# Optimization experiments

Measured on AMD Instinct MI355X. Metric: run time of the kernel, lower is better.

Reference implementation:

```python
import jax, jax.numpy as jnp
import numpy as np

HEADS = 16
DIM_HEAD = 64
SEG = 512        # segment_len (block-diagonal window)
P = 16           # num persistent memory tokens


def rmsnorm(x, g, eps=1e-6):
    var = jnp.mean(x * x, axis=-1, keepdims=True)
    return x * jax.lax.rsqrt(var + eps) * g


def setup_inputs() -> dict:
    key = jax.random.key(0)
    ks = jax.random.split(key, 6)
    B, S, D = 2, 4096, 1024
    inner = HEADS * DIM_HEAD
    return {
        "x": jax.random.normal(ks[0], (B, S, D), jnp.float32),
        "gamma": jnp.ones((D,), jnp.float32),
        "w_qkv": jax.random.normal(ks[1], (D, inner * 3), jnp.float32) * (D ** -0.5),
        "w_out": jax.random.normal(ks[2], (inner, D), jnp.float32) * (inner ** -0.5),
        "pm_k": jax.random.normal(ks[3], (HEADS, P, DIM_HEAD), jnp.float32) * 0.02,
        "pm_v": jax.random.normal(ks[4], (HEADS, P, DIM_HEAD), jnp.float32) * 0.02,
    }


def reference(x, gamma, w_qkv, w_out, pm_k, pm_v):
    # SegmentedAttention forward (MAC block-diagonal causal + persistent memory)
    B, S, D = x.shape
    pad = (-S) % SEG
    Sp = S + pad
    nw = Sp // SEG

    h = rmsnorm(x, gamma)
    qkv = h @ w_qkv                              # [B, S, 3*inner]
    q, k, v = jnp.split(qkv, 3, axis=-1)

    def fold(t):
        # pad and fold segments into batch: b (w n) (h d) -> b w h n d
        t = jnp.pad(t, ((0, 0), (0, pad), (0, 0)))
        t = t.reshape(B, nw, SEG, HEADS, DIM_HEAD)
        return t.transpose(0, 1, 3, 2, 4)        # [B, W, H, SEG, Dh]

    q, k, v = fold(q), fold(k), fold(v)

    # persistent memory tokens prepended to every segment's k/v
    pmk = jnp.broadcast_to(pm_k, (B, nw, HEADS, P, DIM_HEAD))
    pmv = jnp.broadcast_to(pm_v, (B, nw, HEADS, P, DIM_HEAD))
    k = jnp.concatenate([pmk, k], axis=3)        # [B, W, H, P+SEG, Dh]
    v = jnp.concatenate([pmv, v], axis=3)

    scale = DIM_HEAD ** -0.5
    sim = jnp.einsum('bwhid,bwhjd->bwhij', q, k) * scale  # [B,W,H,SEG,P+SEG]

    # mask: persistent mem always visible; within-segment causal (block
    # diagonality is implicit from folding segments into batch)
    qi = jnp.arange(SEG)[:, None]
    kj = jnp.arange(SEG + P)[None, :] - P
    mask = (kj < 0) | (qi >= kj)
    sim = jnp.where(mask, sim, -jnp.inf)

    attn = jax.nn.softmax(sim, axis=-1)
    out = jnp.einsum('bwhij,bwhjd->bwhid', attn, v)       # [B,W,H,SEG,Dh]
    out = out.transpose(0, 1, 3, 2, 4).reshape(B, Sp, HEADS * DIM_HEAD)
    out = out[:, :S]
    return out @ w_out
```

## Files before the change

### kernel.cpp

```cpp
#include <hip/hip_runtime.h>

typedef __attribute__((ext_vector_type(8))) short short8;
typedef __attribute__((ext_vector_type(4))) float float4v;

#define SEG 512
#define PMEM 16
#define NKEY 528

__device__ __forceinline__ float b2f(unsigned int u) {
    union { unsigned int i; float f; } v; v.i = u << 16; return v.f;
}
__device__ __forceinline__ unsigned short f2b(float f) {
    union { float f; unsigned int i; } v; v.f = f;
    unsigned int b = v.i;
    return (unsigned short)((b + 0x7FFFu + ((b >> 16) & 1u)) >> 16);
}

__device__ __forceinline__ int detect_bf16(const void* gamma) {
    return ((const unsigned short*)gamma)[0] == 0x3F80u;
}

__device__ __forceinline__ void async_ld16(const unsigned short* g, unsigned short* l) {
    __builtin_amdgcn_global_load_lds(
        (const __attribute__((address_space(1))) void*)g,
        (__attribute__((address_space(3))) void*)l,
        16, 0, 0);
}

__global__ __launch_bounds__(256) void prep_k(
    const void* __restrict__ w_qkv, const void* __restrict__ w_out,
    const void* __restrict__ pm_k, const void* __restrict__ pm_v,
    const void* __restrict__ x, const void* __restrict__ gamma,
    unsigned short* __restrict__ wqkvT, unsigned short* __restrict__ woutT,
    unsigned short* __restrict__ pmkb, unsigned short* __restrict__ pmvb,
    unsigned short* __restrict__ h) {
    int f = detect_bf16(gamma);
    int bidx = blockIdx.x;
    int tid = threadIdx.x;
    if (bidx < 4096) {
        __shared__ unsigned short t[32][33];
        const void* in; unsigned short* out; int R, C, bx, by;
        if (bidx < 3072) {
            in = w_qkv; out = wqkvT; R = 1024; C = 3072;
            bx = (bidx % 96) * 32; by = (bidx / 96) * 32;
        } else {
            int t2 = bidx - 3072;
            in = w_out; out = woutT; R = 1024; C = 1024;
            bx = (t2 & 31) * 32; by = (t2 >> 5) * 32;
        }
        const unsigned short* in16 = (const unsigned short*)in;
        const float* in32 = (const float*)in;
        int tx = tid & 31, ty = tid >> 5;
        #pragma unroll
        for (int j = 0; j < 32; j += 8) {
            long idx = (long)(by + ty + j) * C + bx + tx;
            t[ty + j][tx] = f ? in16[idx] : f2b(in32[idx]);
        }
        __syncthreads();
        #pragma unroll
        for (int j = 0; j < 32; j += 8)
            out[(long)(bx + ty + j) * R + by + tx] = t[tx][ty + j];
    } else if (bidx < 4104) {
        int i = (bidx - 4096) * 2048 + tid * 8;
        if (f) {
            *(uint4*)(pmkb + i) = *(const uint4*)((const unsigned short*)pm_k + i);
            *(uint4*)(pmvb + i) = *(const uint4*)((const unsigned short*)pm_v + i);
        } else {
            const float* pk = (const float*)pm_k + i;
            const float* pv = (const float*)pm_v + i;
            uint4 kd, vd;
            float4 k0 = *(const float4*)pk, k1 = *(const float4*)(pk + 4);
            float4 v0 = *(const float4*)pv, v1 = *(const float4*)(pv + 4);
            kd.x = (unsigned int)f2b(k0.x) | ((unsigned int)f2b(k0.y) << 16);
            kd.y = (unsigned int)f2b(k0.z) | ((unsigned int)f2b(k0.w) << 16);
            kd.z = (unsigned int)f2b(k1.x) | ((unsigned int)f2b(k1.y) << 16);
            kd.w = (unsigned int)f2b(k1.z) | ((unsigned int)f2b(k1.w) << 16);
            vd.x = (unsigned int)f2b(v0.x) | ((unsigned int)f2b(v0.y) << 16);
            vd.y = (unsigned int)f2b(v0.z) | ((unsigned int)f2b(v0.w) << 16);
            vd.z = (unsigned int)f2b(v1.x) | ((unsigned int)f2b(v1.y) << 16);
            vd.w = (unsigned int)f2b(v1.z) | ((unsigned int)f2b(v1.w) << 16);
            *(uint4*)(pmkb + i) = kd;
            *(uint4*)(pmvb + i) = vd;
        }
    } else {
        __shared__ float wsum[4];
        long row = bidx - 4104;
        float f0, f1, f2, f3, g0, g1, g2, g3;
        if (f) {
            const unsigned short* xp = (const unsigned short*)x;
            const unsigned short* gp = (const unsigned short*)gamma;
            uint2 xv = *(const uint2*)(xp + row * 1024 + tid * 4);
            f0 = b2f(xv.x & 0xffffu); f1 = b2f(xv.x >> 16);
            f2 = b2f(xv.y & 0xffffu); f3 = b2f(xv.y >> 16);
            uint2 gv = *(const uint2*)(gp + tid * 4);
            g0 = b2f(gv.x & 0xffffu); g1 = b2f(gv.x >> 16);
            g2 = b2f(gv.y & 0xffffu); g3 = b2f(gv.y >> 16);
        } else {
            const float* xp = (const float*)x;
            const float* gp = (const float*)gamma;
            float4 xv = *(const float4*)(xp + row * 1024 + tid * 4);
            f0 = xv.x; f1 = xv.y; f2 = xv.z; f3 = xv.w;
            float4 gv = *(const float4*)(gp + tid * 4);
            g0 = gv.x; g1 = gv.y; g2 = gv.z; g3 = gv.w;
        }
        float ss = f0 * f0 + f1 * f1 + f2 * f2 + f3 * f3;
        #pragma unroll
        for (int off = 1; off < 64; off <<= 1) ss += __shfl_xor(ss, off, 64);
        int lane = tid & 63, wv = tid >> 6;
        if (lane == 0) wsum[wv] = ss;
        __syncthreads();
        float tot = wsum[0] + wsum[1] + wsum[2] + wsum[3];
        float sc = rsqrtf(tot * (1.0f / 1024.0f) + 1e-6f);
        uint2 o;
        o.x = (unsigned int)f2b(f0 * sc * g0) | ((unsigned int)f2b(f1 * sc * g1) << 16);
        o.y = (unsigned int)f2b(f2 * sc * g2) | ((unsigned int)f2b(f3 * sc * g3) << 16);
        *(uint2*)(h + row * 1024 + tid * 4) = o;
    }
}

__global__ __launch_bounds__(256, 4) void gemm_bt(
    const unsigned short* __restrict__ A, const unsigned short* __restrict__ Bt,
    void* __restrict__ Cv, int M, int N, int K,
    const void* __restrict__ gamma, int out_mode) {
    __shared__ unsigned short SM[16384];
    unsigned short* As = SM;
    unsigned short* Bs = SM + 8192;
    int out_bf16 = out_mode == 0 ? 1 : detect_bf16(gamma);
    int tid = threadIdx.x;
    int lane = tid & 63, wv = tid >> 6;
    int l15 = lane & 15, quad = lane >> 4;
    int wm = (wv >> 1) * 64, wn = (wv & 1) * 64;
    long m0 = (long)blockIdx.y * 128;
    long n0 = (long)blockIdx.x * 128;

    float4v acc[4][4];
    #pragma unroll
    for (int i = 0; i < 4; ++i)
        #pragma unroll
        for (int j = 0; j < 4; ++j) acc[i][j] = (float4v){0.f, 0.f, 0.f, 0.f};

    int r = tid >> 3;
    int c8 = (((tid & 7) ^ (r & 7)) * 8);
    const unsigned short* Ap = A + (m0 + r) * K + c8;
    const unsigned short* Bp = Bt + (n0 + r) * K + c8;
    unsigned short* Ad = As + tid * 8;
    unsigned short* Bd = Bs + tid * 8;

    int s = l15 & 7;

    for (int k0 = 0; k0 < K; k0 += 64) {
        #pragma unroll
        for (int i = 0; i < 4; ++i) {
            async_ld16(Ap + (long)(32 * i) * K + k0, Ad + i * 2048);
            async_ld16(Bp + (long)(32 * i) * K + k0, Bd + i * 2048);
        }
        __syncthreads();
        #pragma unroll
        for (int ksub = 0; ksub < 2; ++ksub) {
            short8 af[4], bfr[4];
            int v = ksub * 4 + quad;
            #pragma unroll
            for (int mt = 0; mt < 4; ++mt)
                af[mt] = *(const short8*)&As[(wm + mt * 16 + l15) * 64 + ((v ^ s) * 8)];
            #pragma unroll
            for (int nt = 0; nt < 4; ++nt)
                bfr[nt] = *(const short8*)&Bs[(wn + nt * 16 + l15) * 64 + ((v ^ s) * 8)];
            #pragma unroll
            for (int mt = 0; mt < 4; ++mt)
                #pragma unroll
                for (int nt = 0; nt < 4; ++nt)
                    acc[mt][nt] = __builtin_amdgcn_mfma_f32_16x16x32_bf16(af[mt], bfr[nt], acc[mt][nt], 0, 0, 0);
        }
        __syncthreads();
    }

    if (out_bf16) {
        unsigned short* Cs = SM;
        #pragma unroll
        for (int mt = 0; mt < 4; ++mt)
            #pragma unroll
            for (int nt = 0; nt < 4; ++nt)
                #pragma unroll
                for (int rr = 0; rr < 4; ++rr) {
                    int row = wm + mt * 16 + quad * 4 + rr;
                    int col = wn + nt * 16 + l15;
                    int colp = col ^ (((row >> 2) & 7) << 4);
                    Cs[row * 128 + colp] = f2b(acc[mt][nt][rr]);
                }
        __syncthreads();
        unsigned short* C = (unsigned short*)Cv;
        #pragma unroll
        for (int p = 0; p < 8; ++p) {
            int off = (p * 256 + tid) * 8;
            int row = off >> 7;
            int colp = off & 127;
            int col = colp ^ (((row >> 2) & 7) << 4);
            *(uint4*)(C + (m0 + row) * N + n0 + col) = *(const uint4*)&Cs[off];
        }
    } else {
        float* Cf = (float*)SM;
        float* C = (float*)Cv;
        #pragma unroll
        for (int half = 0; half < 2; ++half) {
            if (wm == half * 64) {
                #pragma unroll
                for (int mt = 0; mt < 4; ++mt)
                    #pragma unroll
                    for (int nt = 0; nt < 4; ++nt)
                        #pragma unroll
                        for (int rr = 0; rr < 4; ++rr)
                            Cf[(mt * 16 + quad * 4 + rr) * 128 + wn + nt * 16 + l15] = acc[mt][nt][rr];
            }
            __syncthreads();
            #pragma unroll
            for (int p = 0; p < 8; ++p) {
                int off = (p * 256 + tid) * 4;
                int row = off >> 7;
                int col = off & 127;
                *(float4*)(C + (m0 + half * 64 + row) * N + n0 + col) = *(const float4*)&Cf[off];
            }
            __syncthreads();
        }
    }
}

__global__ __launch_bounds__(256) void attn_k(
    const unsigned short* __restrict__ qkv,
    const unsigned short* __restrict__ pmkb,
    const unsigned short* __restrict__ pmvb,
    unsigned short* __restrict__ outp, int S) {
    __shared__ unsigned short SM[17408];
    unsigned short* Klds = SM;
    unsigned short* Pb   = SM;
    unsigned short* Vt   = SM + 8704;

    int hh = blockIdx.x & 15;
    int w  = blockIdx.x >> 4;
    int b  = blockIdx.y;
    int qt = 7 - blockIdx.z;

    int tid = threadIdx.x;
    int lane = tid & 63, wv = tid >> 6;
    int l15 = lane & 15, quad = lane >> 4;

    long base_row = (long)b * S + (long)w * SEG;
    int i0 = qt * 64 + wv * 16;

    const unsigned short* qp = qkv + (base_row + i0 + l15) * 3072 + hh * 64;
    short8 aq0 = *(const short8*)(qp + quad * 8);
    short8 aq1 = *(const short8*)(qp + 32 + quad * 8);
    #pragma unroll
    for (int u = 0; u < 8; ++u) {
        aq0[u] = (short)f2b(b2f((unsigned short)aq0[u]) * 0.125f);
        aq1[u] = (short)f2b(b2f((unsigned short)aq1[u]) * 0.125f);
    }

    float m_i[4], l_i[4];
    float4v Oacc[4];
    #pragma unroll
    for (int r = 0; r < 4; ++r) { m_i[r] = -1e30f; l_i[r] = 0.f; }
    #pragma unroll
    for (int dt = 0; dt < 4; ++dt) Oacc[dt] = (float4v){0.f, 0.f, 0.f, 0.f};

    int jrow = tid >> 3;
    int cbs = (tid & 7) ^ (jrow & 7);
    int c8 = (tid & 7) * 8;
    int rot = tid & 7;

    unsigned short* Pw = Pb + wv * 2176;

    int ndc = (qt + 3) >> 1;
    for (int dc = 0; dc < ndc; ++dc) {
        #pragma unroll
        for (int i = 0; i < 4; ++i) {
            int j = i * 32 + jrow;
            int jj = dc * 128 + j;
            const unsigned short* src;
            if (jj < PMEM)       src = pmkb + ((long)hh * PMEM + jj) * 64 + cbs * 8;
            else if (jj < NKEY)  src = qkv + (base_row + jj - PMEM) * 3072 + 1024 + hh * 64 + cbs * 8;
            else                 src = pmkb + cbs * 8;
            async_ld16(src, Klds + i * 2048 + tid * 8);
        }
        #pragma unroll
        for (int it = 0; it < 4; ++it) {
            int jl = (tid >> 3) + it * 32;
            int jj = dc * 128 + jl;
            uint4 vd;
            if (jj < PMEM)      vd = *(const uint4*)(pmvb + ((long)hh * PMEM + jj) * 64 + c8);
            else if (jj < NKEY) vd = *(const uint4*)(qkv + (base_row + jj - PMEM) * 3072 + 2048 + hh * 64 + c8);
            else                vd = (uint4){0, 0, 0, 0};
            union { uint4 u; unsigned short s[8]; } vu; vu.u = vd;
            int half = jl >> 6, jl6 = jl & 63;
            int colw = ((jl6 + 8 * rot) & 63) + (half << 6);
            #pragma unroll
            for (int u = 0; u < 8; ++u) Vt[(c8 + u) * 136 + colw] = vu.s[u];
        }
        __syncthreads();

        float4v sc[8];
        #pragma unroll
        for (int jt = 0; jt < 8; ++jt) {
            int j = jt * 16 + l15;
            int sw = j & 7;
            short8 bk0 = *(const short8*)&Klds[j * 64 + ((quad ^ sw) * 8)];
            short8 bk1 = *(const short8*)&Klds[j * 64 + (((quad + 4) ^ sw) * 8)];
            float4v a = (float4v){0.f, 0.f, 0.f, 0.f};
            a = __builtin_amdgcn_mfma_f32_16x16x32_bf16(aq0, bk0, a, 0, 0, 0);
            a = __builtin_amdgcn_mfma_f32_16x16x32_bf16(aq1, bk1, a, 0, 0, 0);
            sc[jt] = a;
        }
        __syncthreads();

        if (dc * 128 + 112 > qt * 64) {
            #pragma unroll
            for (int jt = 0; jt < 8; ++jt) {
                int jg = dc * 128 + jt * 16 + l15;
                #pragma unroll
                for (int r = 0; r < 4; ++r) {
                    int i = i0 + quad * 4 + r;
                    bool ok = (jg < PMEM) || ((jg < NKEY) && (i >= jg - PMEM));
                    sc[jt][r] = ok ? sc[jt][r] : -1e30f;
                }
            }
        }
        #pragma unroll
        for (int r = 0; r < 4; ++r) {
            float tmax = fmaxf(fmaxf(fmaxf(sc[0][r], sc[1][r]), fmaxf(sc[2][r], sc[3][r])),
                               fmaxf(fmaxf(sc[4][r], sc[5][r]), fmaxf(sc[6][r], sc[7][r])));
            #pragma unroll
            for (int off = 1; off < 16; off <<= 1)
                tmax = fmaxf(tmax, __shfl_xor(tmax, off, 64));
            float mnew = fmaxf(m_i[r], tmax);
            float alpha = __expf(m_i[r] - mnew);
            float psum = 0.f;
            #pragma unroll
            for (int jt = 0; jt < 8; ++jt) {
                float p = __expf(sc[jt][r] - mnew);
                sc[jt][r] = p;
                psum += p;
            }
            #pragma unroll
            for (int off = 1; off < 16; off <<= 1)
                psum += __shfl_xor(psum, off, 64);
            l_i[r] = l_i[r] * alpha + psum;
            m_i[r] = mnew;
            #pragma unroll
            for (int dt = 0; dt < 4; ++dt) Oacc[dt][r] *= alpha;
        }
        #pragma unroll
        for (int jt = 0; jt < 8; ++jt)
            #pragma unroll
            for (int r = 0; r < 4; ++r)
                Pw[(quad * 4 + r) * 136 + jt * 16 + l15] = f2b(sc[jt][r]);

        short8 ap[4];
        #pragma unroll
        for (int kt = 0; kt < 4; ++kt)
            ap[kt] = *(const short8*)&Pw[l15 * 136 + kt * 32 + quad * 8];

        #pragma unroll
        for (int dt = 0; dt < 4; ++dt) {
            int d = dt * 16 + l15;
            int rb = (d >> 3) & 7;
            #pragma unroll
            for (int kt = 0; kt < 4; ++kt) {
                int k0b = kt * 32 + quad * 8;
                int half = k0b >> 6, j6 = k0b & 63;
                int col = ((j6 + rb * 8) & 63) + (half << 6);
                short8 bv = *(const short8*)&Vt[d * 136 + col];
                Oacc[dt] = __builtin_amdgcn_mfma_f32_16x16x32_bf16(ap[kt], bv, Oacc[dt], 0, 0, 0);
            }
        }
        __syncthreads();
    }

    #pragma unroll
    for (int dt = 0; dt < 4; ++dt)
        #pragma unroll
        for (int r = 0; r < 4; ++r) {
            int i = i0 + quad * 4 + r;
            outp[(base_row + i) * 1024 + hh * 64 + dt * 16 + l15] = f2b(Oacc[dt][r] / l_i[r]);
        }
}

extern "C" void kernel_launch(void* const* d_in, const int* in_sizes, int n_in,
                              void* d_out, int out_size, void* d_ws, size_t ws_size,
                              hipStream_t stream) {
    const void* x     = d_in[0];
    const void* gamma = d_in[1];
    const void* w_qkv = d_in[2];
    const void* w_out = d_in[3];
    const void* pmk   = d_in[4];
    const void* pmv   = d_in[5];

    const int D = 1024, S = 4096;
    const int B = in_sizes[0] / (S * D);
    const long BS = (long)B * S;

    unsigned short* h     = (unsigned short*)d_ws;
    unsigned short* qkvb  = h + BS * 1024;
    unsigned short* wqkvT = qkvb + BS * 3072;
    unsigned short* woutT = wqkvT + (long)3072 * 1024;
    unsigned short* pmkb  = woutT + (long)1024 * 1024;
    unsigned short* pmvb  = pmkb + 16384;
    unsigned short* aout  = h;

    prep_k<<<4104 + (int)BS, 256, 0, stream>>>(w_qkv, w_out, pmk, pmv, x, gamma,
                                               wqkvT, woutT, pmkb, pmvb, h);

    gemm_bt<<<dim3(3072 / 128, (int)(BS / 128)), 256, 0, stream>>>(h, wqkvT, qkvb, (int)BS, 3072, 1024, gamma, 0);

    attn_k<<<dim3(128, B, 8), 256, 0, stream>>>(qkvb, pmkb, pmvb, aout, S);

    gemm_bt<<<dim3(1024 / 128, (int)(BS / 128)), 256, 0, stream>>>(aout, woutT, d_out, (int)BS, 1024, 1024, gamma, 1);
}
```

Measured before the change: 225.5 us.

## Double attention query tile per block to share K/V loads across eight waves

The attention kernel now uses 512 threads (8 waves) covering 128 query rows per block instead of 64, halving the z-grid so each K/V chunk loaded into LDS serves twice as many queries. K, V and P get separate LDS regions, which removes the sync between the QK and PV phases, and the P staging is split into two 64-key halves. Softmax switches to exp2 with log2(e) folded into the query scale. Larger blocks cut global/LDS load traffic per query, but lower the block count and raise LDS use per block, which can reduce occupancy. Causal imbalance across tiles also gets coarser.

```diff
diff --git a/kernel.cpp b/kernel.cpp
--- a/kernel.cpp
+++ b/kernel.cpp
@@ -224,35 +224,35 @@
     }
 }
 
-__global__ __launch_bounds__(256) void attn_k(
+__global__ __launch_bounds__(512) void attn_k(
     const unsigned short* __restrict__ qkv,
     const unsigned short* __restrict__ pmkb,
     const unsigned short* __restrict__ pmvb,
     unsigned short* __restrict__ outp, int S) {
-    __shared__ unsigned short SM[17408];
+    __shared__ unsigned short SM[26112];
     unsigned short* Klds = SM;
-    unsigned short* Pb   = SM;
-    unsigned short* Vt   = SM + 8704;
+    unsigned short* Vt   = SM + 8192;
+    unsigned short* Pb   = SM + 16896;
 
     int hh = blockIdx.x & 15;
     int w  = blockIdx.x >> 4;
     int b  = blockIdx.y;
-    int qt = 7 - blockIdx.z;
+    int qt2 = 3 - blockIdx.z;
 
     int tid = threadIdx.x;
     int lane = tid & 63, wv = tid >> 6;
     int l15 = lane & 15, quad = lane >> 4;
 
     long base_row = (long)b * S + (long)w * SEG;
-    int i0 = qt * 64 + wv * 16;
+    int i0 = qt2 * 128 + wv * 16;
 
     const unsigned short* qp = qkv + (base_row + i0 + l15) * 3072 + hh * 64;
     short8 aq0 = *(const short8*)(qp + quad * 8);
     short8 aq1 = *(const short8*)(qp + 32 + quad * 8);
     #pragma unroll
     for (int u = 0; u < 8; ++u) {
-        aq0[u] = (short)f2b(b2f((unsigned short)aq0[u]) * 0.125f);
-        aq1[u] = (short)f2b(b2f((unsigned short)aq1[u]) * 0.125f);
+        aq0[u] = (short)f2b(b2f((unsigned short)aq0[u]) * 0.18033688f);
+        aq1[u] = (short)f2b(b2f((unsigned short)aq1[u]) * 0.18033688f);
     }
 
     float m_i[4], l_i[4];
@@ -267,31 +267,30 @@
     int c8 = (tid & 7) * 8;
     int rot = tid & 7;
 
-    unsigned short* Pw = Pb + wv * 2176;
-
-    int ndc = (qt + 3) >> 1;
+    unsigned short* Pw = Pb + wv * 1152;
+
+    int ndc = qt2 + 2;
     for (int dc = 0; dc < ndc; ++dc) {
         #pragma unroll
-        for (int i = 0; i < 4; ++i) {
-            int j = i * 32 + jrow;
-            int jj = dc * 128 + j;
+        for (int it = 0; it < 2; ++it) {
+            int jj = dc * 128 + it * 64 + jrow;
             const unsigned short* src;
             if (jj < PMEM)       src = pmkb + ((long)hh * PMEM + jj) * 64 + cbs * 8;
             else if (jj < NKEY)  src = qkv + (base_row + jj - PMEM) * 3072 + 1024 + hh * 64 + cbs * 8;
             else                 src = pmkb + cbs * 8;
-            async_ld16(src, Klds + i * 2048 + tid * 8);
-        }
-        #pragma unroll
-        for (int it = 0; it < 4; ++it) {
-            int jl = (tid >> 3) + it * 32;
+            async_ld16(src, Klds + it * 4096 + tid * 8);
+        }
+        #pragma unroll
+        for (int it = 0; it < 2; ++it) {
+            int jl = it * 64 + jrow;
             int jj = dc * 128 + jl;
             uint4 vd;
             if (jj < PMEM)      vd = *(const uint4*)(pmvb + ((long)hh * PMEM + jj) * 64 + c8);
             else if (jj < NKEY) vd = *(const uint4*)(qkv + (base_row + jj - PMEM) * 3072 + 2048 + hh * 64 + c8);
             else                vd = (uint4){0, 0, 0, 0};
             union { uint4 u; unsigned short s[8]; } vu; vu.u = vd;
-            int half = jl >> 6, jl6 = jl & 63;
-            int colw = ((jl6 + 8 * rot) & 63) + (half << 6);
+            int jl6 = jl & 63;
+            int colw = ((jl6 + 8 * rot) & 63) + (it << 6);
             #pragma unroll
             for (int u = 0; u < 8; ++u) Vt[(c8 + u) * 136 + colw] = vu.s[u];
         }
@@ -309,9 +308,8 @@
             a = __builtin_amdgcn_mfma_f32_16x16x32_bf16(aq1, bk1, a, 0, 0, 0);
             sc[jt] = a;
         }
-        __syncthreads();
-
-        if (dc * 128 + 112 > qt * 64) {
+
+        if (dc * 128 + 111 > i0) {
             #pragma unroll
             for (int jt = 0; jt < 8; ++jt) {
                 int jg = dc * 128 + jt * 16 + l15;
@@ -331,11 +329,11 @@
             for (int off = 1; off < 16; off <<= 1)
                 tmax = fmaxf(tmax, __shfl_xor(tmax, off, 64));
             float mnew = fmaxf(m_i[r], tmax);
-            float alpha = __expf(m_i[r] - mnew);
+            float alpha = exp2f(m_i[r] - mnew);
             float psum = 0.f;
             #pragma unroll
             for (int jt = 0; jt < 8; ++jt) {
-                float p = __expf(sc[jt][r] - mnew);
+                float p = exp2f(sc[jt][r] - mnew);
                 sc[jt][r] = p;
                 psum += p;
             }
@@ -348,27 +346,27 @@
             for (int dt = 0; dt < 4; ++dt) Oacc[dt][r] *= alpha;
         }
         #pragma unroll
-        for (int jt = 0; jt < 8; ++jt)
-            #pragma unroll
-            for (int r = 0; r < 4; ++r)
-                Pw[(quad * 4 + r) * 136 + jt * 16 + l15] = f2b(sc[jt][r]);
-
-        short8 ap[4];
-        #pragma unroll
-        for (int kt = 0; kt < 4; ++kt)
-            ap[kt] = *(const short8*)&Pw[l15 * 136 + kt * 32 + quad * 8];
-
-        #pragma unroll
-        for (int dt = 0; dt < 4; ++dt) {
-            int d = dt * 16 + l15;
-            int rb = (d >> 3) & 7;
-            #pragma unroll
-            for (int kt = 0; kt < 4; ++kt) {
-                int k0b = kt * 32 + quad * 8;
-                int half = k0b >> 6, j6 = k0b & 63;
-                int col = ((j6 + rb * 8) & 63) + (half << 6);
-                short8 bv = *(const short8*)&Vt[d * 136 + col];
-                Oacc[dt] = __builtin_amdgcn_mfma_f32_16x16x32_bf16(ap[kt], bv, Oacc[dt], 0, 0, 0);
+        for (int ph = 0; ph < 2; ++ph) {
+            #pragma unroll
+            for (int jt = 0; jt < 4; ++jt)
+                #pragma unroll
+                for (int r = 0; r < 4; ++r)
+                    Pw[(quad * 4 + r) * 72 + jt * 16 + l15] = f2b(sc[ph * 4 + jt][r]);
+            short8 ap[2];
+            #pragma unroll
+            for (int kt = 0; kt < 2; ++kt)
+                ap[kt] = *(const short8*)&Pw[l15 * 72 + kt * 32 + quad * 8];
+            #pragma unroll
+            for (int dt = 0; dt < 4; ++dt) {
+                int d = dt * 16 + l15;
+                int rb = (d >> 3) & 7;
+                #pragma unroll
+                for (int kt = 0; kt < 2; ++kt) {
+                    int j6 = kt * 32 + quad * 8;
+                    int col = ((j6 + rb * 8) & 63) + (ph << 6);
+                    short8 bv = *(const short8*)&Vt[d * 136 + col];
+                    Oacc[dt] = __builtin_amdgcn_mfma_f32_16x16x32_bf16(ap[kt], bv, Oacc[dt], 0, 0, 0);
+                }
             }
         }
         __syncthreads();
@@ -410,7 +408,7 @@
 
     gemm_bt<<<dim3(3072 / 128, (int)(BS / 128)), 256, 0, stream>>>(h, wqkvT, qkvb, (int)BS, 3072, 1024, gamma, 0);
 
-    attn_k<<<dim3(128, B, 8), 256, 0, stream>>>(qkvb, pmkb, pmvb, aout, S);
+    attn_k<<<dim3(128, B, 4), 512, 0, stream>>>(qkvb, pmkb, pmvb, aout, S);
 
     gemm_bt<<<dim3(1024 / 128, (int)(BS / 128)), 256, 0, stream>>>(aout, woutT, d_out, (int)BS, 1024, 1024, gamma, 1);
 }
```

Result: slower. 238.4 us (+5.7%).
